# Performance work log

Measured on AMD Instinct MI355X. Metric: run time of the kernel, lower is better.

Reference implementation:

```python
import jax, jax.numpy as jnp
import numpy as np

B, D, T, H = 1024, 128, 256, 64  # batch, input_dim, seq_len, hidden_dim


def _lstm_layer(x_proj, w_hh):
    """x_proj: [B, T, 4H] precomputed input projection (incl. both biases).
    Returns (all hidden states [B, T, H], final hidden [B, H])."""
    b = x_proj.shape[0]
    h0 = jnp.zeros((b, H), x_proj.dtype)
    c0 = jnp.zeros((b, H), x_proj.dtype)

    def step(carry, xt):
        h, c = carry
        gates = xt + h @ w_hh.T  # [B, 4H]; PyTorch gate order i, f, g, o
        i, f, g, o = jnp.split(gates, 4, axis=-1)
        i = jax.nn.sigmoid(i)
        f = jax.nn.sigmoid(f)
        g = jnp.tanh(g)
        o = jax.nn.sigmoid(o)
        c = f * c + i * g
        h = o * jnp.tanh(c)
        return (h, c), h

    (hT, _), ys = jax.lax.scan(step, (h0, c0), x_proj.transpose(1, 0, 2))
    return ys.transpose(1, 0, 2), hT


def setup_inputs() -> dict:
    key = jax.random.key(0)
    ks = jax.random.split(key, 11)
    s = 1.0 / np.sqrt(H)  # PyTorch LSTM init scale
    return {
        "x": jax.random.normal(ks[0], (B, D, T), jnp.float32),
        "w_ih0": jax.random.normal(ks[1], (4 * H, D), jnp.float32) * s,
        "w_hh0": jax.random.normal(ks[2], (4 * H, H), jnp.float32) * s,
        "b_ih0": jax.random.normal(ks[3], (4 * H,), jnp.float32) * s,
        "b_hh0": jax.random.normal(ks[4], (4 * H,), jnp.float32) * s,
        "w_ih1": jax.random.normal(ks[5], (4 * H, H), jnp.float32) * s,
        "w_hh1": jax.random.normal(ks[6], (4 * H, H), jnp.float32) * s,
        "b_ih1": jax.random.normal(ks[7], (4 * H,), jnp.float32) * s,
        "b_hh1": jax.random.normal(ks[8], (4 * H,), jnp.float32) * s,
        "w_fc": jax.random.normal(ks[9], (D, H), jnp.float32) * s,
        "b_fc": jax.random.normal(ks[10], (D,), jnp.float32) * s,
    }


def reference(x, w_ih0, w_hh0, b_ih0, b_hh0, w_ih1, w_hh1, b_ih1, b_hh1, w_fc, b_fc):
    # x: [B, input_dim, T] -> permute(0, 2, 1) -> [B, T, input_dim]
    xt = x.transpose(0, 2, 1)
    # Layer 0: precompute input projection for all timesteps (one big GEMM)
    xp0 = xt @ w_ih0.T + (b_ih0 + b_hh0)  # [B, T, 4H]
    ys0, _ = _lstm_layer(xp0, w_hh0)
    # Inter-layer dropout(p=0.3) is identity in eval/inference mode.
    xp1 = ys0 @ w_ih1.T + (b_ih1 + b_hh1)  # [B, T, 4H]
    _, hT = _lstm_layer(xp1, w_hh1)
    # Final-timestep linear head: lstm_out[:, -1, :] == final hidden state hT
    scores = hT @ w_fc.T + b_fc  # [B, input_dim]
    return scores
```

## Files before the change

### kernel.cpp

```cpp
#include <hip/hip_runtime.h>

#define PH  72
#define HSZ 1152
#define XRW 144
#define XSL 584

typedef float f32x4 __attribute__((ext_vector_type(4)));
typedef _Float16 f16x8 __attribute__((ext_vector_type(8)));

__device__ __forceinline__ float sigmoid_f(float x) {
    float e = __builtin_amdgcn_exp2f(-1.4426950408889634f * x);
    return __builtin_amdgcn_rcpf(1.0f + e);
}
__device__ __forceinline__ float tanh_f(float x) {
    float e = __builtin_amdgcn_exp2f(-2.8853900817779268f * x);
    return 2.0f * __builtin_amdgcn_rcpf(1.0f + e) - 1.0f;
}
__device__ __forceinline__ f16x8 load_frag16h(const float* wp, int n, int K, int k0) {
    const float* wf = wp + (size_t)n * K + k0;
    f16x8 h;
    #pragma unroll
    for (int j = 0; j < 8; ++j) h[j] = (_Float16)wf[j];
    return h;
}
__device__ __forceinline__ void gload16(const void* g, void* l) {
    __builtin_amdgcn_global_load_lds(
        (const __attribute__((address_space(1))) unsigned int*)g,
        (__attribute__((address_space(3))) unsigned int*)l, 16, 0, 0);
}

#define MFMA16(a, b, c) __builtin_amdgcn_mfma_f32_16x16x32_f16(a, b, c, 0, 0, 0)

__global__ __launch_bounds__(768, 3) void rec_fused(
    const float* __restrict__ x,
    const float* __restrict__ wih0, const float* __restrict__ whh0,
    const float* __restrict__ bih0, const float* __restrict__ bhh0,
    const float* __restrict__ wih1, const float* __restrict__ whh1,
    const float* __restrict__ bih1, const float* __restrict__ bhh1,
    const float* __restrict__ wfc,  const float* __restrict__ bfc,
    float* __restrict__ out)
{
    __shared__ float    xs32[4 * 2048];
    __shared__ _Float16 xh[32 * XSL];
    __shared__ float    xpl[4 * 1024];
    __shared__ _Float16 h0[2 * HSZ], h1[2 * HSZ];
    const int tid = threadIdx.x, lane = tid & 63, w = tid >> 6;
    const int l16 = lane & 15, quad = lane >> 4, k0 = quad * 8;
    const int wl = w & 3;
    const int role = w >> 2;
    const bool is1 = (role == 0), is0 = (role == 1), isP = (role == 2);
    const int bb  = blockIdx.x & 63;
    const int sub = blockIdx.x >> 6;

    const float* xrow = x + (size_t)(bb * 16 + wl * 4 + sub) * 128 * 256;

    f16x8 fA[4][2], fB[4][4];
    float gb[4] = {0.f, 0.f, 0.f, 0.f};
    #pragma unroll
    for (int g = 0; g < 4; ++g) {
        const int n = g * 64 + wl * 16 + l16;
        if (is1) {
            #pragma unroll
            for (int ks = 0; ks < 2; ++ks) {
                fA[g][ks] = load_frag16h(wih1, n, 64, ks * 32 + k0);
                fB[g][ks] = load_frag16h(whh1, n, 64, ks * 32 + k0);
            }
            gb[g] = bih1[n] + bhh1[n];
        } else if (is0) {
            #pragma unroll
            for (int ks = 0; ks < 2; ++ks)
                fA[g][ks] = load_frag16h(whh0, n, 64, ks * 32 + k0);
        } else {
            #pragma unroll
            for (int ks = 0; ks < 4; ++ks)
                fB[g][ks] = load_frag16h(wih0, n, 128, ks * 32 + k0);
            gb[g] = bih0[n] + bhh0[n];
        }
    }
    for (int i = tid; i < 2 * HSZ; i += 768) { h0[i] = (_Float16)0.f; h1[i] = (_Float16)0.f; }
    float c = 0.f;

    auto convert_rows = [&](int cc, int ib0, int nib) {
        const int sb = (cc & 1) * 16;
        const int tq = lane & 3;
        for (int ib = ib0; ib < ib0 + nib; ++ib) {
            const float4 v = *(const float4*)&xs32[wl * 2048 + ib * 256 + lane * 4];
            const int d = ib * 16 + (lane >> 2);
            const float vv[4] = {v.x, v.y, v.z, v.w};
            #pragma unroll
            for (int j = 0; j < 4; ++j)
                xh[(sb + tq * 4 + j) * XSL + wl * XRW + d] = (_Float16)vv[j];
        }
    };
    auto issue_chunk = [&](int cc) {
        #pragma unroll
        for (int ib = 0; ib < 8; ++ib)
            gload16(xrow + (size_t)(ib * 16 + (lane >> 2)) * 256 + cc * 16 + (lane & 3) * 4,
                    (char*)xs32 + wl * 8192 + ib * 1024);
    };
    auto compute_xp = [&](int tp) {
        const int fs = ((tp >> 4) & 1) * 16 + (tp & 15);
        f16x8 ax[4];
        #pragma unroll
        for (int ks = 0; ks < 4; ++ks)
            ax[ks] = *(const f16x8*)&xh[fs * XSL + (l16 >> 2) * XRW + ks * 32 + k0];
        f32x4 pa[4];
        #pragma unroll
        for (int g = 0; g < 4; ++g) pa[g] = (f32x4){gb[g], 0.f, 0.f, 0.f};
        #pragma unroll
        for (int g = 0; g < 4; ++g)
            #pragma unroll
            for (int ks = 0; ks < 4; ++ks)
                pa[g] = MFMA16(ax[ks], fB[g][ks], pa[g]);
        f32x4 o;
        o[0] = pa[0][0]; o[1] = pa[1][0]; o[2] = pa[2][0]; o[3] = pa[3][0];
        *(f32x4*)&xpl[(((tp & 3) * 4 + wl) * 64 + lane) * 4] = o;
    };
    auto store_h = [&](_Float16* hbuf, int slot, float hv) {
        const _Float16 hh = (_Float16)hv;
        const int base = slot * HSZ + (quad * 4) * PH + wl * 16 + l16;
        hbuf[base]      = hh;
        hbuf[base + PH] = (_Float16)(hv - (float)hh);
    };

    if (isP) issue_chunk(0);
    __syncthreads();
    if (isP) { convert_rows(0, 0, 8); issue_chunk(1); }
    __syncthreads();
    if (isP) { compute_xp(0); compute_xp(1); compute_xp(2); }
    __syncthreads();
    if (is0) {
        const f32x4 xp4 = *(const f32x4*)&xpl[(wl * 64 + lane) * 4];
        const float gi = sigmoid_f(xp4[0]);
        const float gg = tanh_f(xp4[2]);
        const float go = sigmoid_f(xp4[3]);
        c = gi * gg;
        store_h(h0, 0, go * tanh_f(c));
    }
    __syncthreads();

    for (int t = 0; t < 255; ++t) {
        const int s0 = t & 1, s1 = s0 ^ 1;
        const int tn = t + 1;
        if (is1) {
            f16x8 ah[2], bh[2];
            #pragma unroll
            for (int ks = 0; ks < 2; ++ks) {
                ah[ks] = *(const f16x8*)&h0[s0 * HSZ + l16 * PH + ks * 32 + k0];
                bh[ks] = *(const f16x8*)&h1[s1 * HSZ + l16 * PH + ks * 32 + k0];
            }
            f32x4 acc[4];
            #pragma unroll
            for (int g = 0; g < 4; ++g)
                acc[g] = (f32x4){gb[g], 0.f, 0.f, 0.f};
            #pragma unroll
            for (int g = 0; g < 4; ++g)
                #pragma unroll
                for (int ks = 0; ks < 2; ++ks) {
                    acc[g] = MFMA16(ah[ks], fA[g][ks], acc[g]);
                    acc[g] = MFMA16(bh[ks], fB[g][ks], acc[g]);
                }
            const float gi = sigmoid_f(acc[0][0] + acc[0][1]);
            const float gf = sigmoid_f(acc[1][0] + acc[1][1]);
            const float gg = tanh_f(acc[2][0] + acc[2][1]);
            const float go = sigmoid_f(acc[3][0] + acc[3][1]);
            c = gf * c + gi * gg;
            store_h(h1, s0, go * tanh_f(c));
        } else if (is0) {
            const f32x4 xp4 =
                *(const f32x4*)&xpl[(((tn & 3) * 4 + wl) * 64 + lane) * 4];
            f16x8 ah[2];
            #pragma unroll
            for (int ks = 0; ks < 2; ++ks)
                ah[ks] = *(const f16x8*)&h0[s0 * HSZ + l16 * PH + ks * 32 + k0];
            f32x4 acc[4];
            #pragma unroll
            for (int g = 0; g < 4; ++g)
                acc[g] = (f32x4){xp4[g], 0.f, 0.f, 0.f};
            #pragma unroll
            for (int g = 0; g < 4; ++g)
                #pragma unroll
                for (int ks = 0; ks < 2; ++ks)
                    acc[g] = MFMA16(ah[ks], fA[g][ks], acc[g]);
            const float gi = sigmoid_f(acc[0][0] + acc[0][1]);
            const float gf = sigmoid_f(acc[1][0] + acc[1][1]);
            const float gg = tanh_f(acc[2][0] + acc[2][1]);
            const float go = sigmoid_f(acc[3][0] + acc[3][1]);
            c = gf * c + gi * gg;
            store_h(h0, s1, go * tanh_f(c));
        } else {
            const int tp = t + 3;
            if (tp <= 255) compute_xp(tp);
            if ((tn & 15) == 0 && tn < 240)
                issue_chunk((tn >> 4) + 1);
            const int m16 = tn & 15;
            if (m16 >= 8 && m16 < 12 && tn < 248)
                convert_rows((tn >> 4) + 1, (m16 - 8) * 2, 2);
        }
        __syncthreads();
    }

    if (is1) {
        f16x8 ah[2], bh[2];
        #pragma unroll
        for (int ks = 0; ks < 2; ++ks) {
            ah[ks] = *(const f16x8*)&h0[HSZ + l16 * PH + ks * 32 + k0];
            bh[ks] = *(const f16x8*)&h1[l16 * PH + ks * 32 + k0];
        }
        f32x4 acc[4];
        #pragma unroll
        for (int g = 0; g < 4; ++g)
            acc[g] = (f32x4){gb[g], 0.f, 0.f, 0.f};
        #pragma unroll
        for (int g = 0; g < 4; ++g)
            #pragma unroll
            for (int ks = 0; ks < 2; ++ks) {
                acc[g] = MFMA16(ah[ks], fA[g][ks], acc[g]);
                acc[g] = MFMA16(bh[ks], fB[g][ks], acc[g]);
            }
        const float gi = sigmoid_f(acc[0][0] + acc[0][1]);
        const float gf = sigmoid_f(acc[1][0] + acc[1][1]);
        const float gg = tanh_f(acc[2][0] + acc[2][1]);
        const float go = sigmoid_f(acc[3][0] + acc[3][1]);
        c = gf * c + gi * gg;
        store_h(h1, 1, go * tanh_f(c));
    }
    __syncthreads();

    if (tid < 512) {
        const int n   = tid & 127;
        const int sel = tid >> 7;
        float s = 0.f;
        for (int k = 0; k < 64; ++k)
            s += ((float)h1[HSZ + (sel * 4) * PH + k]
                + (float)h1[HSZ + (sel * 4 + 1) * PH + k]) * wfc[n * 64 + k];
        out[(size_t)(bb * 16 + sel * 4 + sub) * 128 + n] = s + bfc[n];
    }
}

extern "C" void kernel_launch(void* const* d_in, const int* in_sizes, int n_in,
                              void* d_out, int out_size, void* d_ws, size_t ws_size,
                              hipStream_t stream) {
    const float* x     = (const float*)d_in[0];
    const float* wih0  = (const float*)d_in[1];
    const float* whh0  = (const float*)d_in[2];
    const float* bih0  = (const float*)d_in[3];
    const float* bhh0  = (const float*)d_in[4];
    const float* wih1  = (const float*)d_in[5];
    const float* whh1  = (const float*)d_in[6];
    const float* bih1  = (const float*)d_in[7];
    const float* bhh1  = (const float*)d_in[8];
    const float* wfc   = (const float*)d_in[9];
    const float* bfc   = (const float*)d_in[10];
    float* out = (float*)d_out;

    rec_fused<<<256, 768, 0, stream>>>(x, wih0, whh0, bih0, bhh0,
                                       wih1, whh1, bih1, bhh1, wfc, bfc, out);
}
```

Before: 348.8 us.

## Batch layer-0 input projection across four timesteps per MFMA pass

The producer waves used to compute the input projection one timestep at a time, using only one row of each 16x16 MFMA output. They now pack four timesteps into the MFMA rows, computing four steps of projections per call every fourth iteration into an 8-slot ring buffer. Chunk load and convert scheduling is moved to fit the new cadence. This cuts the producer's MFMA work by about four times, but puts a burst of work on every fourth step, which could lengthen those barrier intervals. Shared memory use also grows.

```diff
diff --git a/kernel.cpp b/kernel.cpp
--- a/kernel.cpp
+++ b/kernel.cpp
@@ -42,7 +42,7 @@
 {
     __shared__ float    xs32[4 * 2048];
     __shared__ _Float16 xh[32 * XSL];
-    __shared__ float    xpl[4 * 1024];
+    __shared__ float    xpl[8 * 1024];
     __shared__ _Float16 h0[2 * HSZ], h1[2 * HSZ];
     const int tid = threadIdx.x, lane = tid & 63, w = tid >> 6;
     const int l16 = lane & 15, quad = lane >> 4, k0 = quad * 8;
@@ -98,23 +98,23 @@
             gload16(xrow + (size_t)(ib * 16 + (lane >> 2)) * 256 + cc * 16 + (lane & 3) * 4,
                     (char*)xs32 + wl * 8192 + ib * 1024);
     };
-    auto compute_xp = [&](int tp) {
-        const int fs = ((tp >> 4) & 1) * 16 + (tp & 15);
+    auto compute_xp4 = [&](int tb) {
+        const int tpl = tb + (l16 & 3);
+        const int fs  = ((tpl >> 4) & 1) * 16 + (tpl & 15);
         f16x8 ax[4];
         #pragma unroll
         for (int ks = 0; ks < 4; ++ks)
             ax[ks] = *(const f16x8*)&xh[fs * XSL + (l16 >> 2) * XRW + ks * 32 + k0];
-        f32x4 pa[4];
-        #pragma unroll
-        for (int g = 0; g < 4; ++g) pa[g] = (f32x4){gb[g], 0.f, 0.f, 0.f};
-        #pragma unroll
-        for (int g = 0; g < 4; ++g)
+        #pragma unroll
+        for (int g = 0; g < 4; ++g) {
+            f32x4 pa = (f32x4){gb[g], gb[g], gb[g], gb[g]};
             #pragma unroll
             for (int ks = 0; ks < 4; ++ks)
-                pa[g] = MFMA16(ax[ks], fB[g][ks], pa[g]);
-        f32x4 o;
-        o[0] = pa[0][0]; o[1] = pa[1][0]; o[2] = pa[2][0]; o[3] = pa[3][0];
-        *(f32x4*)&xpl[(((tp & 3) * 4 + wl) * 64 + lane) * 4] = o;
+                pa = MFMA16(ax[ks], fB[g][ks], pa);
+            #pragma unroll
+            for (int r = 0; r < 4; ++r)
+                xpl[((((tb + r) & 7) * 4 + wl) * 64 + lane) * 4 + g] = pa[r];
+        }
     };
     auto store_h = [&](_Float16* hbuf, int slot, float hv) {
         const _Float16 hh = (_Float16)hv;
@@ -125,9 +125,9 @@
 
     if (isP) issue_chunk(0);
     __syncthreads();
-    if (isP) { convert_rows(0, 0, 8); issue_chunk(1); }
-    __syncthreads();
-    if (isP) { compute_xp(0); compute_xp(1); compute_xp(2); }
+    if (isP) convert_rows(0, 0, 8);
+    __syncthreads();
+    if (isP) compute_xp4(0);
     __syncthreads();
     if (is0) {
         const f32x4 xp4 = *(const f32x4*)&xpl[(wl * 64 + lane) * 4];
@@ -168,7 +168,7 @@
             store_h(h1, s0, go * tanh_f(c));
         } else if (is0) {
             const f32x4 xp4 =
-                *(const f32x4*)&xpl[(((tn & 3) * 4 + wl) * 64 + lane) * 4];
+                *(const f32x4*)&xpl[(((tn & 7) * 4 + wl) * 64 + lane) * 4];
             f16x8 ah[2];
             #pragma unroll
             for (int ks = 0; ks < 2; ++ks)
@@ -189,13 +189,13 @@
             c = gf * c + gi * gg;
             store_h(h0, s1, go * tanh_f(c));
         } else {
-            const int tp = t + 3;
-            if (tp <= 255) compute_xp(tp);
-            if ((tn & 15) == 0 && tn < 240)
-                issue_chunk((tn >> 4) + 1);
-            const int m16 = tn & 15;
-            if (m16 >= 8 && m16 < 12 && tn < 248)
-                convert_rows((tn >> 4) + 1, (m16 - 8) * 2, 2);
+            if ((t & 3) == 0 && t <= 248)
+                compute_xp4(t + 4);
+            if ((t & 15) == 1 && t < 240)
+                issue_chunk((t >> 4) + 1);
+            const int m16 = t & 15;
+            if (m16 >= 4 && m16 < 8 && t < 240)
+                convert_rows((t >> 4) + 1, (m16 - 4) * 2, 2);
         }
         __syncthreads();
     }
```

Result: slower. 358.7 us (+2.8%).

## Fold layer-0 input projection into recurrent warps and drop producer warps

Applied to the files above, without the earlier changes.

Removes the separate producer warp group that computed the layer-0 input projection three steps ahead into a shared buffer. The layer-0 warps now run the input-projection MFMAs inline each step, reading the fp16 x tile directly, and also handle the x chunk loads and conversion. The block shrinks from 768 to 512 threads and the xpl buffer is gone. In exchange, the layer-0 critical path per step gains extra MFMAs and the loads, which may lengthen the serial recurrence.

```diff
diff --git a/kernel.cpp b/kernel.cpp
--- a/kernel.cpp
+++ b/kernel.cpp
@@ -31,7 +31,7 @@
 
 #define MFMA16(a, b, c) __builtin_amdgcn_mfma_f32_16x16x32_f16(a, b, c, 0, 0, 0)
 
-__global__ __launch_bounds__(768, 3) void rec_fused(
+__global__ __launch_bounds__(512, 2) void rec_fused(
     const float* __restrict__ x,
     const float* __restrict__ wih0, const float* __restrict__ whh0,
     const float* __restrict__ bih0, const float* __restrict__ bhh0,
@@ -42,20 +42,18 @@
 {
     __shared__ float    xs32[4 * 2048];
     __shared__ _Float16 xh[32 * XSL];
-    __shared__ float    xpl[4 * 1024];
     __shared__ _Float16 h0[2 * HSZ], h1[2 * HSZ];
     const int tid = threadIdx.x, lane = tid & 63, w = tid >> 6;
     const int l16 = lane & 15, quad = lane >> 4, k0 = quad * 8;
     const int wl = w & 3;
-    const int role = w >> 2;
-    const bool is1 = (role == 0), is0 = (role == 1), isP = (role == 2);
+    const bool is1 = (w < 4);
     const int bb  = blockIdx.x & 63;
     const int sub = blockIdx.x >> 6;
 
     const float* xrow = x + (size_t)(bb * 16 + wl * 4 + sub) * 128 * 256;
 
     f16x8 fA[4][2], fB[4][4];
-    float gb[4] = {0.f, 0.f, 0.f, 0.f};
+    float gb[4];
     #pragma unroll
     for (int g = 0; g < 4; ++g) {
         const int n = g * 64 + wl * 16 + l16;
@@ -66,18 +64,17 @@
                 fB[g][ks] = load_frag16h(whh1, n, 64, ks * 32 + k0);
             }
             gb[g] = bih1[n] + bhh1[n];
-        } else if (is0) {
+        } else {
+            #pragma unroll
+            for (int ks = 0; ks < 4; ++ks)
+                fB[g][ks] = load_frag16h(wih0, n, 128, ks * 32 + k0);
             #pragma unroll
             for (int ks = 0; ks < 2; ++ks)
                 fA[g][ks] = load_frag16h(whh0, n, 64, ks * 32 + k0);
-        } else {
-            #pragma unroll
-            for (int ks = 0; ks < 4; ++ks)
-                fB[g][ks] = load_frag16h(wih0, n, 128, ks * 32 + k0);
             gb[g] = bih0[n] + bhh0[n];
         }
     }
-    for (int i = tid; i < 2 * HSZ; i += 768) { h0[i] = (_Float16)0.f; h1[i] = (_Float16)0.f; }
+    for (int i = tid; i < 2 * HSZ; i += 512) { h0[i] = (_Float16)0.f; h1[i] = (_Float16)0.f; }
     float c = 0.f;
 
     auto convert_rows = [&](int cc, int ib0, int nib) {
@@ -98,24 +95,6 @@
             gload16(xrow + (size_t)(ib * 16 + (lane >> 2)) * 256 + cc * 16 + (lane & 3) * 4,
                     (char*)xs32 + wl * 8192 + ib * 1024);
     };
-    auto compute_xp = [&](int tp) {
-        const int fs = ((tp >> 4) & 1) * 16 + (tp & 15);
-        f16x8 ax[4];
-        #pragma unroll
-        for (int ks = 0; ks < 4; ++ks)
-            ax[ks] = *(const f16x8*)&xh[fs * XSL + (l16 >> 2) * XRW + ks * 32 + k0];
-        f32x4 pa[4];
-        #pragma unroll
-        for (int g = 0; g < 4; ++g) pa[g] = (f32x4){gb[g], 0.f, 0.f, 0.f};
-        #pragma unroll
-        for (int g = 0; g < 4; ++g)
-            #pragma unroll
-            for (int ks = 0; ks < 4; ++ks)
-                pa[g] = MFMA16(ax[ks], fB[g][ks], pa[g]);
-        f32x4 o;
-        o[0] = pa[0][0]; o[1] = pa[1][0]; o[2] = pa[2][0]; o[3] = pa[3][0];
-        *(f32x4*)&xpl[(((tp & 3) * 4 + wl) * 64 + lane) * 4] = o;
-    };
     auto store_h = [&](_Float16* hbuf, int slot, float hv) {
         const _Float16 hh = (_Float16)hv;
         const int base = slot * HSZ + (quad * 4) * PH + wl * 16 + l16;
@@ -123,17 +102,27 @@
         hbuf[base + PH] = (_Float16)(hv - (float)hh);
     };
 
-    if (isP) issue_chunk(0);
-    __syncthreads();
-    if (isP) { convert_rows(0, 0, 8); issue_chunk(1); }
-    __syncthreads();
-    if (isP) { compute_xp(0); compute_xp(1); compute_xp(2); }
-    __syncthreads();
-    if (is0) {
-        const f32x4 xp4 = *(const f32x4*)&xpl[(wl * 64 + lane) * 4];
-        const float gi = sigmoid_f(xp4[0]);
-        const float gg = tanh_f(xp4[2]);
-        const float go = sigmoid_f(xp4[3]);
+    if (!is1) issue_chunk(0);
+    __syncthreads();
+    if (!is1) { convert_rows(0, 0, 8); issue_chunk(1); }
+    __syncthreads();
+
+    if (!is1) {
+        f16x8 ax[4];
+        #pragma unroll
+        for (int ks = 0; ks < 4; ++ks)
+            ax[ks] = *(const f16x8*)&xh[(l16 >> 2) * XRW + ks * 32 + k0];
+        f32x4 accA[4];
+        #pragma unroll
+        for (int g = 0; g < 4; ++g) accA[g] = (f32x4){gb[g], gb[g], gb[g], gb[g]};
+        #pragma unroll
+        for (int g = 0; g < 4; ++g)
+            #pragma unroll
+            for (int ks = 0; ks < 4; ++ks)
+                accA[g] = MFMA16(ax[ks], fB[g][ks], accA[g]);
+        const float gi = sigmoid_f(accA[0][0]);
+        const float gg = tanh_f(accA[2][0]);
+        const float go = sigmoid_f(accA[3][0]);
         c = gi * gg;
         store_h(h0, 0, go * tanh_f(c));
     }
@@ -166,31 +155,36 @@
             const float go = sigmoid_f(acc[3][0] + acc[3][1]);
             c = gf * c + gi * gg;
             store_h(h1, s0, go * tanh_f(c));
-        } else if (is0) {
-            const f32x4 xp4 =
-                *(const f32x4*)&xpl[(((tn & 3) * 4 + wl) * 64 + lane) * 4];
-            f16x8 ah[2];
+        } else {
+            const int slot = tn & 31;
+            f16x8 ax[4], ah[2];
+            #pragma unroll
+            for (int ks = 0; ks < 4; ++ks)
+                ax[ks] = *(const f16x8*)&xh[slot * XSL + (l16 >> 2) * XRW + ks * 32 + k0];
             #pragma unroll
             for (int ks = 0; ks < 2; ++ks)
                 ah[ks] = *(const f16x8*)&h0[s0 * HSZ + l16 * PH + ks * 32 + k0];
-            f32x4 acc[4];
-            #pragma unroll
-            for (int g = 0; g < 4; ++g)
-                acc[g] = (f32x4){xp4[g], 0.f, 0.f, 0.f};
-            #pragma unroll
-            for (int g = 0; g < 4; ++g)
+            f32x4 accA[4], accB[4];
+            #pragma unroll
+            for (int g = 0; g < 4; ++g) {
+                accA[g] = (f32x4){gb[g], 0.f, 0.f, 0.f};
+                accB[g] = (f32x4){0.f, 0.f, 0.f, 0.f};
+            }
+            #pragma unroll
+            for (int g = 0; g < 4; ++g) {
+                #pragma unroll
+                for (int ks = 0; ks < 4; ++ks)
+                    accA[g] = MFMA16(ax[ks], fB[g][ks], accA[g]);
                 #pragma unroll
                 for (int ks = 0; ks < 2; ++ks)
-                    acc[g] = MFMA16(ah[ks], fA[g][ks], acc[g]);
-            const float gi = sigmoid_f(acc[0][0] + acc[0][1]);
-            const float gf = sigmoid_f(acc[1][0] + acc[1][1]);
-            const float gg = tanh_f(acc[2][0] + acc[2][1]);
-            const float go = sigmoid_f(acc[3][0] + acc[3][1]);
+                    accB[g] = MFMA16(ah[ks], fA[g][ks], accB[g]);
+            }
+            const float gi = sigmoid_f(accA[0][0] + accB[0][0] + accB[0][1]);
+            const float gf = sigmoid_f(accA[1][0] + accB[1][0] + accB[1][1]);
+            const float gg = tanh_f(accA[2][0] + accB[2][0] + accB[2][1]);
+            const float go = sigmoid_f(accA[3][0] + accB[3][0] + accB[3][1]);
             c = gf * c + gi * gg;
             store_h(h0, s1, go * tanh_f(c));
-        } else {
-            const int tp = t + 3;
-            if (tp <= 255) compute_xp(tp);
             if ((tn & 15) == 0 && tn < 240)
                 issue_chunk((tn >> 4) + 1);
             const int m16 = tn & 15;
@@ -227,15 +221,13 @@
     }
     __syncthreads();
 
-    if (tid < 512) {
-        const int n   = tid & 127;
-        const int sel = tid >> 7;
-        float s = 0.f;
-        for (int k = 0; k < 64; ++k)
-            s += ((float)h1[HSZ + (sel * 4) * PH + k]
-                + (float)h1[HSZ + (sel * 4 + 1) * PH + k]) * wfc[n * 64 + k];
-        out[(size_t)(bb * 16 + sel * 4 + sub) * 128 + n] = s + bfc[n];
-    }
+    const int n   = tid & 127;
+    const int sel = tid >> 7;
+    float s = 0.f;
+    for (int k = 0; k < 64; ++k)
+        s += ((float)h1[HSZ + (sel * 4) * PH + k]
+            + (float)h1[HSZ + (sel * 4 + 1) * PH + k]) * wfc[n * 64 + k];
+    out[(size_t)(bb * 16 + sel * 4 + sub) * 128 + n] = s + bfc[n];
 }
 
 extern "C" void kernel_launch(void* const* d_in, const int* in_sizes, int n_in,
@@ -254,6 +246,6 @@
     const float* bfc   = (const float*)d_in[10];
     float* out = (float*)d_out;
 
-    rec_fused<<<256, 768, 0, stream>>>(x, wih0, whh0, bih0, bhh0,
+    rec_fused<<<256, 512, 0, stream>>>(x, wih0, whh0, bih0, bhh0,
                                        wih1, whh1, bih1, bhh1, wfc, bfc, out);
 }
```

Measured after the change: 362.6 us. +4.0%, slower.
